# Kernel optimization log

Hardware: AMD Instinct MI355X
Metric: run time of the kernel (lower is better)

## Reference

```python
import jax, jax.numpy as jnp
import numpy as np

D_IN = 1024
D_OUT = 1024
H = 16


def setup_inputs() -> dict:
    key = jax.random.key(0)
    ks = jax.random.split(key, 11)
    B, Tq, Tk = 2, 2048, 2048
    s = 1.0 / np.sqrt(D_IN)
    return {
        "q": jax.random.normal(ks[0], (B, Tq, D_IN), jnp.float32),
        "k": jax.random.normal(ks[1], (B, Tk, D_IN), jnp.float32),
        "v": jax.random.normal(ks[2], (B, Tk, D_IN), jnp.float32),
        "Wq": jax.random.uniform(ks[3], (D_IN, D_OUT), jnp.float32, -s, s),
        "bq": jax.random.uniform(ks[4], (D_OUT,), jnp.float32, -s, s),
        "Wk": jax.random.uniform(ks[5], (D_IN, D_OUT), jnp.float32, -s, s),
        "bk": jax.random.uniform(ks[6], (D_OUT,), jnp.float32, -s, s),
        "Wv": jax.random.uniform(ks[7], (D_IN, D_OUT), jnp.float32, -s, s),
        "bv": jax.random.uniform(ks[8], (D_OUT,), jnp.float32, -s, s),
        "Wo": jax.random.uniform(ks[9], (D_OUT, D_OUT), jnp.float32, -s, s),
        "bo": jax.random.uniform(ks[10], (D_OUT,), jnp.float32, -s, s),
    }


def reference(q, k, v, Wq, bq, Wk, bk, Wv, bv, Wo, bo):
    B, Tq, _ = q.shape
    Tk = k.shape[1]
    hd = D_OUT // H
    # QKV projections, split heads -> [B, H, T, hd]
    qh = (q @ Wq + bq).reshape(B, Tq, H, hd).transpose(0, 2, 1, 3)
    kh = (k @ Wk + bk).reshape(B, Tk, H, hd).transpose(0, 2, 1, 3)
    vh = (v @ Wv + bv).reshape(B, Tk, H, hd).transpose(0, 2, 1, 3)
    # scaled dot-product attention (scale uses key dim = head_dim)
    scores = jnp.einsum("bhqd,bhkd->bhqk", qh, kh) / jnp.sqrt(jnp.float32(hd))
    attn = jax.nn.softmax(scores, axis=-1)
    x = jnp.einsum("bhqk,bhkd->bhqd", attn, vh)
    x = x.transpose(0, 2, 1, 3).reshape(B, Tq, D_OUT)
    return x @ Wo + bo
```

## Files before the change

kernel.cpp:

```cpp
#include <hip/hip_runtime.h>
#include <hip/hip_bf16.h>

typedef __attribute__((ext_vector_type(8))) short short8;
typedef __attribute__((ext_vector_type(4))) short short4v;
typedef __attribute__((ext_vector_type(4))) float f32x4;

__device__ __forceinline__ unsigned short f2bf(float f) {
    __hip_bfloat16 h = __float2bfloat16(f);
    unsigned short u;
    __builtin_memcpy(&u, &h, 2);
    return u;
}
__device__ __forceinline__ short4v pack4bf(float a, float b, float c, float d) {
    union { unsigned u[2]; short4v s; } r;
    r.u[0] = ((unsigned)f2bf(b) << 16) | f2bf(a);
    r.u[1] = ((unsigned)f2bf(d) << 16) | f2bf(c);
    return r.s;
}

#define GLD16(gp, lp) __builtin_amdgcn_global_load_lds( \
    (const __attribute__((address_space(1))) void*)(gp), \
    (__attribute__((address_space(3))) void*)(lp), 16, 0, 0)

__global__ __launch_bounds__(256) void prep(
    const float* __restrict__ q, const float* __restrict__ k, const float* __restrict__ v,
    unsigned short* __restrict__ qb, unsigned short* __restrict__ kb, unsigned short* __restrict__ vb,
    const float* __restrict__ W0, const float* __restrict__ W1,
    const float* __restrict__ W2, const float* __restrict__ W3,
    unsigned short* __restrict__ T0, unsigned short* __restrict__ T1,
    unsigned short* __restrict__ T2, unsigned short* __restrict__ T3)
{
    __shared__ unsigned short Ts[64 * 72];
    int bx = blockIdx.x;
    if (bx < 6144) {
        const float* src; unsigned short* dst;
        switch (bx >> 11) { case 0: src = q; dst = qb; break;
                            case 1: src = k; dst = kb; break;
                            default: src = v; dst = vb; break; }
        size_t i = ((size_t)(bx & 2047) * 256 + threadIdx.x) * 8;
        float4 x0 = *(const float4*)&src[i];
        float4 x1 = *(const float4*)&src[i + 4];
        union { unsigned short s[8]; uint4 u; } p;
        p.s[0] = f2bf(x0.x); p.s[1] = f2bf(x0.y); p.s[2] = f2bf(x0.z); p.s[3] = f2bf(x0.w);
        p.s[4] = f2bf(x1.x); p.s[5] = f2bf(x1.y); p.s[6] = f2bf(x1.z); p.s[7] = f2bf(x1.w);
        *(uint4*)&dst[i] = p.u;
        return;
    }
    int w = bx - 6144;
    int z = w >> 8, rem = w & 255;
    int kx = rem >> 4, ny = rem & 15;
    const float* W;
    unsigned short* T;
    switch (z) {
        case 0: W = W0; T = T0; break;
        case 1: W = W1; T = T1; break;
        case 2: W = W2; T = T2; break;
        default: W = W3; T = T3; break;
    }
    int tid = threadIdx.x;
    int c = tid & 7, r = tid >> 3;
    int k0 = kx * 64, n0 = ny * 64;
    for (int i = 0; i < 64; i += 32) {
        const float* src = &W[(size_t)(k0 + r + i) * 1024 + n0 + c * 8];
        float4 x0 = *(const float4*)src;
        float4 x1 = *(const float4*)(src + 4);
        unsigned short* d = &Ts[(r + i) * 72 + c * 8];
        d[0] = f2bf(x0.x); d[1] = f2bf(x0.y); d[2] = f2bf(x0.z); d[3] = f2bf(x0.w);
        d[4] = f2bf(x1.x); d[5] = f2bf(x1.y); d[6] = f2bf(x1.z); d[7] = f2bf(x1.w);
    }
    __syncthreads();
    for (int i = 0; i < 64; i += 32) {
        union { unsigned short s[8]; uint4 v; } u;
        for (int j = 0; j < 8; j++) u.s[j] = Ts[(c * 8 + j) * 72 + (r + i)];
        *(uint4*)&T[(size_t)(n0 + r + i) * 1024 + k0 + c * 8] = u.v;
    }
}

__device__ __forceinline__ void gemm_core(
    const unsigned short* __restrict__ A, const unsigned short* __restrict__ BT,
    const float* __restrict__ bias, void* __restrict__ outv,
    int mode, float scale)
{
    const int K = 1024;
    __shared__ unsigned short As[128 * 32];
    __shared__ unsigned short Bs[128 * 32];
    int tid = threadIdx.x;
    int m0 = blockIdx.x * 128, n0 = blockIdx.y * 128;
    int lane = tid & 63, wave = tid >> 6;
    int lm = lane & 15, quad = lane >> 4;
    int wm = (wave >> 1) * 64, wn = (wave & 1) * 64;

    int lrow = lane >> 2;
    int scol = ((lane & 3) ^ ((lane >> 3) & 3)) * 8;
    const unsigned short* Ag = A + (size_t)(m0 + wave * 32 + lrow) * K + scol;
    const unsigned short* Bg = BT + (size_t)(n0 + wave * 32 + lrow) * K + scol;
    unsigned short* AsW0 = &As[(wave * 32) * 32];
    unsigned short* AsW1 = &As[(wave * 32 + 16) * 32];
    unsigned short* BsW0 = &Bs[(wave * 32) * 32];
    unsigned short* BsW1 = &Bs[(wave * 32 + 16) * 32];

    int rpos = (quad ^ ((lm >> 1) & 3)) * 8;

    f32x4 acc[4][4];
    for (int i = 0; i < 4; i++)
        for (int j = 0; j < 4; j++)
            for (int r = 0; r < 4; r++) acc[i][j][r] = 0.0f;

    for (int kb = 0; kb < K; kb += 32) {
        GLD16(Ag, AsW0);
        GLD16(Ag + 16 * K, AsW1);
        GLD16(Bg, BsW0);
        GLD16(Bg + 16 * K, BsW1);
        Ag += 32; Bg += 32;
        __syncthreads();
        short8 a[4], b[4];
        for (int i = 0; i < 4; i++)
            a[i] = *(const short8*)&As[(wm + i * 16 + lm) * 32 + rpos];
        for (int j = 0; j < 4; j++)
            b[j] = *(const short8*)&Bs[(wn + j * 16 + lm) * 32 + rpos];
        for (int i = 0; i < 4; i++)
            for (int j = 0; j < 4; j++)
                acc[i][j] = __builtin_amdgcn_mfma_f32_16x16x32_bf16(a[i], b[j], acc[i][j], 0, 0, 0);
        __syncthreads();
    }

    for (int j = 0; j < 4; j++) {
        int col = n0 + wn + j * 16 + lm;
        float bv = bias[col];
        for (int i = 0; i < 4; i++) {
            int rowb = m0 + wm + i * 16 + quad * 4;
            if (mode == 0) {
                float* out32 = (float*)outv;
                for (int r = 0; r < 4; r++)
                    out32[(size_t)(rowb + r) * 1024 + col] = (acc[i][j][r] + bv) * scale;
            } else if (mode == 1) {
                unsigned short* out16 = (unsigned short*)outv;
                int h = col >> 6, d = col & 63;
                int bb = rowb >> 11, t = rowb & 2047;
                size_t base = (((size_t)(bb * 16 + h)) * 2048 + t) * 64 + d;
                for (int r = 0; r < 4; r++)
                    out16[base + (size_t)r * 64] = f2bf((acc[i][j][r] + bv) * scale);
            } else {
                unsigned short* out16 = (unsigned short*)outv;
                int h = col >> 6, d = col & 63;
                int bb = rowb >> 11, t = rowb & 2047;
                ushort4 pk;
                pk.x = f2bf((acc[i][j][0] + bv) * scale);
                pk.y = f2bf((acc[i][j][1] + bv) * scale);
                pk.z = f2bf((acc[i][j][2] + bv) * scale);
                pk.w = f2bf((acc[i][j][3] + bv) * scale);
                *(ushort4*)&out16[(((size_t)(bb * 16 + h)) * 64 + d) * 2048 + t] = pk;
            }
        }
    }
}

__global__ __launch_bounds__(256) void qkv_gemm(
    const unsigned short* __restrict__ qbf, const unsigned short* __restrict__ kbf,
    const unsigned short* __restrict__ vbf,
    const unsigned short* __restrict__ WqT, const unsigned short* __restrict__ WkT,
    const unsigned short* __restrict__ WvT,
    const float* __restrict__ bq, const float* __restrict__ bk, const float* __restrict__ bv,
    unsigned short* __restrict__ Qh, unsigned short* __restrict__ Kh,
    unsigned short* __restrict__ VhT)
{
    switch (blockIdx.z) {
        case 0:  gemm_core(qbf, WqT, bq, Qh,  1, 0.18033688011f); break;
        case 1:  gemm_core(kbf, WkT, bk, Kh,  1, 1.0f);           break;
        default: gemm_core(vbf, WvT, bv, VhT, 2, 1.0f);           break;
    }
}

__global__ __launch_bounds__(256) void out_gemm(
    const unsigned short* __restrict__ X, const unsigned short* __restrict__ WoT,
    const float* __restrict__ bo, float* __restrict__ out)
{
    gemm_core(X, WoT, bo, out, 0, 1.0f);
}

__global__ __launch_bounds__(256) void attn_kernel(
    const unsigned short* __restrict__ Qh, const unsigned short* __restrict__ Kh,
    const unsigned short* __restrict__ VhT, unsigned short* __restrict__ X)
{
    __shared__ unsigned short Ks[2][64 * 64];
    __shared__ unsigned short Vt[2][64 * 64];

    int tid = threadIdx.x;
    int qb = blockIdx.x & 31, bh = blockIdx.x >> 5;
    int b = bh >> 4, h = bh & 15;
    int lane = tid & 63, wave = tid >> 6;
    int lm = lane & 15, quad = lane >> 4;

    const unsigned short* Kbase = Kh + (size_t)bh * 2048 * 64;
    const unsigned short* Vbase = VhT + (size_t)bh * 64 * 2048;

    int srow = wave * 8 + (lane >> 3);
    int schk = ((lane & 7) ^ ((lane >> 3) & 7)) * 8;
    int swz  = lm & 7;
    int c0 = (quad ^ swz) * 8;
    int c1 = ((quad + 4) ^ swz) * 8;

    int qrow = qb * 64 + wave * 16 + lm;
    const unsigned short* qptr = Qh + ((size_t)bh * 2048 + qrow) * 64;
    short8 qf0 = *(const short8*)&qptr[quad * 8];
    short8 qf1 = *(const short8*)&qptr[32 + quad * 8];

    f32x4 o[4];
    for (int n = 0; n < 4; n++)
        for (int r = 0; r < 4; r++) o[n][r] = 0.0f;
    float l = 0.0f;

    GLD16(&Kbase[(size_t)srow * 64 + schk],          &Ks[0][(wave * 8) * 64]);
    GLD16(&Kbase[(size_t)(32 + srow) * 64 + schk],   &Ks[0][(32 + wave * 8) * 64]);
    GLD16(&Vbase[(size_t)srow * 2048 + schk],        &Vt[0][(wave * 8) * 64]);
    GLD16(&Vbase[(size_t)(32 + srow) * 2048 + schk], &Vt[0][(32 + wave * 8) * 64]);
    __syncthreads();

    for (int kt = 0; kt < 32; kt++) {
        int cur = kt & 1;
        if (kt < 31) {
            int k1 = (kt + 1) * 64;
            int nxt = cur ^ 1;
            GLD16(&Kbase[(size_t)(k1 + srow) * 64 + schk],        &Ks[nxt][(wave * 8) * 64]);
            GLD16(&Kbase[(size_t)(k1 + 32 + srow) * 64 + schk],   &Ks[nxt][(32 + wave * 8) * 64]);
            GLD16(&Vbase[(size_t)srow * 2048 + k1 + schk],        &Vt[nxt][(wave * 8) * 64]);
            GLD16(&Vbase[(size_t)(32 + srow) * 2048 + k1 + schk], &Vt[nxt][(32 + wave * 8) * 64]);
        }

        short4v pa[4];
        for (int t = 0; t < 4; t++) {
            short8 ka0 = *(const short8*)&Ks[cur][(t * 16 + lm) * 64 + c0];
            short8 ka1 = *(const short8*)&Ks[cur][(t * 16 + lm) * 64 + c1];
            f32x4 z;
            z[0] = z[1] = z[2] = z[3] = 0.0f;
            z = __builtin_amdgcn_mfma_f32_16x16x32_bf16(ka0, qf0, z, 0, 0, 0);
            z = __builtin_amdgcn_mfma_f32_16x16x32_bf16(ka1, qf1, z, 0, 0, 0);
            float p0 = __builtin_amdgcn_exp2f(z[0]);
            float p1 = __builtin_amdgcn_exp2f(z[1]);
            float p2 = __builtin_amdgcn_exp2f(z[2]);
            float p3 = __builtin_amdgcn_exp2f(z[3]);
            l += (p0 + p1) + (p2 + p3);
            pa[t] = pack4bf(p0, p1, p2, p3);
        }

        int wo = (quad & 1) * 4;
        for (int n = 0; n < 4; n++) {
            int rbase = (n * 16 + lm) * 64;
            for (int t = 0; t < 4; t++) {
                int chunk = t * 2 + (quad >> 1);
                short4v vb = *(const short4v*)&Vt[cur][rbase + ((chunk ^ swz) * 8) + wo];
                o[n] = __builtin_amdgcn_mfma_f32_16x16x16bf16_1k(pa[t], vb, o[n], 0, 0, 0);
            }
        }
        __syncthreads();
    }

    l += __shfl_xor(l, 16);
    l += __shfl_xor(l, 32);
    float inv = 1.0f / l;

    for (int r = 0; r < 4; r++) {
        float invr = __shfl(inv, (lane & 48) | (quad * 4 + r));
        int row = qb * 64 + wave * 16 + quad * 4 + r;
        for (int n = 0; n < 4; n++)
            X[((size_t)b * 2048 + row) * 1024 + h * 64 + n * 16 + lm] = f2bf(o[n][r] * invr);
    }
}

extern "C" void kernel_launch(void* const* d_in, const int* in_sizes, int n_in,
                              void* d_out, int out_size, void* d_ws, size_t ws_size,
                              hipStream_t stream)
{
    const float* q  = (const float*)d_in[0];
    const float* k  = (const float*)d_in[1];
    const float* v  = (const float*)d_in[2];
    const float* Wq = (const float*)d_in[3];
    const float* bq = (const float*)d_in[4];
    const float* Wk = (const float*)d_in[5];
    const float* bk = (const float*)d_in[6];
    const float* Wv = (const float*)d_in[7];
    const float* bv = (const float*)d_in[8];
    const float* Wo = (const float*)d_in[9];
    const float* bo = (const float*)d_in[10];

    unsigned short* ws  = (unsigned short*)d_ws;
    const unsigned int M1 = 1u << 20;
    unsigned short* WqT = ws;
    unsigned short* WkT = ws + M1;
    unsigned short* WvT = ws + 2 * M1;
    unsigned short* WoT = ws + 3 * M1;
    unsigned short* qbf = ws + 4 * M1;
    unsigned short* kbf = ws + 8 * M1;
    unsigned short* vbf = ws + 12 * M1;
    unsigned short* Qh  = ws + 16 * M1;
    unsigned short* Kh  = ws + 4 * M1;
    unsigned short* VhT = ws + 8 * M1;
    unsigned short* X   = ws + 12 * M1;

    prep<<<dim3(7168), 256, 0, stream>>>(q, k, v, qbf, kbf, vbf,
                                         Wq, Wk, Wv, Wo, WqT, WkT, WvT, WoT);
    qkv_gemm<<<dim3(32, 8, 3), 256, 0, stream>>>(qbf, kbf, vbf, WqT, WkT, WvT,
                                                 bq, bk, bv, Qh, Kh, VhT);
    attn_kernel<<<dim3(1024), 256, 0, stream>>>(Qh, Kh, VhT, X);
    out_gemm<<<dim3(32, 8), 256, 0, stream>>>(X, WoT, bo, (float*)d_out);
}
```

Baseline: 235.6 us.

## Double per-wave query rows in attention and vectorize GEMM epilogue stores

The attention kernel now handles 128 query rows per block (32 per wave, as two 16-row sub-tiles), so each K/V tile loaded into shared memory is reused across twice as many queries and the grid is halved. Separately, the GEMM swaps MFMA operand order for modes 0 and 1 so each lane holds four consecutive columns. That lets the epilogue use float4 bias loads and float4/ushort4 vector stores instead of scalar strided stores. The cost is more registers per wave in attention and fewer blocks to fill the GPU.

After: 252.1 us. 7.0% more time.

```diff
diff --git a/kernel.cpp b/kernel.cpp
--- a/kernel.cpp
+++ b/kernel.cpp
@@ -118,30 +118,57 @@
             a[i] = *(const short8*)&As[(wm + i * 16 + lm) * 32 + rpos];
         for (int j = 0; j < 4; j++)
             b[j] = *(const short8*)&Bs[(wn + j * 16 + lm) * 32 + rpos];
-        for (int i = 0; i < 4; i++)
-            for (int j = 0; j < 4; j++)
-                acc[i][j] = __builtin_amdgcn_mfma_f32_16x16x32_bf16(a[i], b[j], acc[i][j], 0, 0, 0);
+        if (mode == 2) {
+            for (int i = 0; i < 4; i++)
+                for (int j = 0; j < 4; j++)
+                    acc[i][j] = __builtin_amdgcn_mfma_f32_16x16x32_bf16(a[i], b[j], acc[i][j], 0, 0, 0);
+        } else {
+            for (int i = 0; i < 4; i++)
+                for (int j = 0; j < 4; j++)
+                    acc[i][j] = __builtin_amdgcn_mfma_f32_16x16x32_bf16(b[j], a[i], acc[i][j], 0, 0, 0);
+        }
         __syncthreads();
     }
 
-    for (int j = 0; j < 4; j++) {
-        int col = n0 + wn + j * 16 + lm;
-        float bv = bias[col];
-        for (int i = 0; i < 4; i++) {
-            int rowb = m0 + wm + i * 16 + quad * 4;
-            if (mode == 0) {
-                float* out32 = (float*)outv;
-                for (int r = 0; r < 4; r++)
-                    out32[(size_t)(rowb + r) * 1024 + col] = (acc[i][j][r] + bv) * scale;
-            } else if (mode == 1) {
-                unsigned short* out16 = (unsigned short*)outv;
-                int h = col >> 6, d = col & 63;
-                int bb = rowb >> 11, t = rowb & 2047;
-                size_t base = (((size_t)(bb * 16 + h)) * 2048 + t) * 64 + d;
-                for (int r = 0; r < 4; r++)
-                    out16[base + (size_t)r * 64] = f2bf((acc[i][j][r] + bv) * scale);
-            } else {
-                unsigned short* out16 = (unsigned short*)outv;
+    if (mode == 0) {
+        float* out32 = (float*)outv;
+        for (int j = 0; j < 4; j++) {
+            int cbase = n0 + wn + j * 16 + quad * 4;
+            float4 b4 = *(const float4*)&bias[cbase];
+            for (int i = 0; i < 4; i++) {
+                int row = m0 + wm + i * 16 + lm;
+                float4 st;
+                st.x = (acc[i][j][0] + b4.x) * scale;
+                st.y = (acc[i][j][1] + b4.y) * scale;
+                st.z = (acc[i][j][2] + b4.z) * scale;
+                st.w = (acc[i][j][3] + b4.w) * scale;
+                *(float4*)&out32[(size_t)row * 1024 + cbase] = st;
+            }
+        }
+    } else if (mode == 1) {
+        unsigned short* out16 = (unsigned short*)outv;
+        for (int j = 0; j < 4; j++) {
+            int cbase = n0 + wn + j * 16 + quad * 4;
+            float4 b4 = *(const float4*)&bias[cbase];
+            int h = cbase >> 6, d0 = cbase & 63;
+            for (int i = 0; i < 4; i++) {
+                int rowm = m0 + wm + i * 16 + lm;
+                int bb = rowm >> 11, t = rowm & 2047;
+                ushort4 pk;
+                pk.x = f2bf((acc[i][j][0] + b4.x) * scale);
+                pk.y = f2bf((acc[i][j][1] + b4.y) * scale);
+                pk.z = f2bf((acc[i][j][2] + b4.z) * scale);
+                pk.w = f2bf((acc[i][j][3] + b4.w) * scale);
+                *(ushort4*)&out16[(((size_t)(bb * 16 + h)) * 2048 + t) * 64 + d0] = pk;
+            }
+        }
+    } else {
+        unsigned short* out16 = (unsigned short*)outv;
+        for (int j = 0; j < 4; j++) {
+            int col = n0 + wn + j * 16 + lm;
+            float bv = bias[col];
+            for (int i = 0; i < 4; i++) {
+                int rowb = m0 + wm + i * 16 + quad * 4;
                 int h = col >> 6, d = col & 63;
                 int bb = rowb >> 11, t = rowb & 2047;
                 ushort4 pk;
@@ -186,7 +213,7 @@
     __shared__ unsigned short Vt[2][64 * 64];
 
     int tid = threadIdx.x;
-    int qb = blockIdx.x & 31, bh = blockIdx.x >> 5;
+    int qb = blockIdx.x & 15, bh = blockIdx.x >> 4;
     int b = bh >> 4, h = bh & 15;
     int lane = tid & 63, wave = tid >> 6;
     int lm = lane & 15, quad = lane >> 4;
@@ -200,15 +227,20 @@
     int c0 = (quad ^ swz) * 8;
     int c1 = ((quad + 4) ^ swz) * 8;
 
-    int qrow = qb * 64 + wave * 16 + lm;
-    const unsigned short* qptr = Qh + ((size_t)bh * 2048 + qrow) * 64;
-    short8 qf0 = *(const short8*)&qptr[quad * 8];
-    short8 qf1 = *(const short8*)&qptr[32 + quad * 8];
-
-    f32x4 o[4];
-    for (int n = 0; n < 4; n++)
-        for (int r = 0; r < 4; r++) o[n][r] = 0.0f;
-    float l = 0.0f;
+    int qrow = qb * 128 + wave * 32 + lm;
+    const unsigned short* qptr0 = Qh + ((size_t)bh * 2048 + qrow) * 64;
+    const unsigned short* qptr1 = qptr0 + 16 * 64;
+    short8 qf[2][2];
+    qf[0][0] = *(const short8*)&qptr0[quad * 8];
+    qf[0][1] = *(const short8*)&qptr0[32 + quad * 8];
+    qf[1][0] = *(const short8*)&qptr1[quad * 8];
+    qf[1][1] = *(const short8*)&qptr1[32 + quad * 8];
+
+    f32x4 o[2][4];
+    for (int qs = 0; qs < 2; qs++)
+        for (int n = 0; n < 4; n++)
+            for (int r = 0; r < 4; r++) o[qs][n][r] = 0.0f;
+    float lsum[2] = {0.0f, 0.0f};
 
     GLD16(&Kbase[(size_t)srow * 64 + schk],          &Ks[0][(wave * 8) * 64]);
     GLD16(&Kbase[(size_t)(32 + srow) * 64 + schk],   &Ks[0][(32 + wave * 8) * 64]);
@@ -227,20 +259,22 @@
             GLD16(&Vbase[(size_t)(32 + srow) * 2048 + k1 + schk], &Vt[nxt][(32 + wave * 8) * 64]);
         }
 
-        short4v pa[4];
+        short4v pa[2][4];
         for (int t = 0; t < 4; t++) {
             short8 ka0 = *(const short8*)&Ks[cur][(t * 16 + lm) * 64 + c0];
             short8 ka1 = *(const short8*)&Ks[cur][(t * 16 + lm) * 64 + c1];
-            f32x4 z;
-            z[0] = z[1] = z[2] = z[3] = 0.0f;
-            z = __builtin_amdgcn_mfma_f32_16x16x32_bf16(ka0, qf0, z, 0, 0, 0);
-            z = __builtin_amdgcn_mfma_f32_16x16x32_bf16(ka1, qf1, z, 0, 0, 0);
-            float p0 = __builtin_amdgcn_exp2f(z[0]);
-            float p1 = __builtin_amdgcn_exp2f(z[1]);
-            float p2 = __builtin_amdgcn_exp2f(z[2]);
-            float p3 = __builtin_amdgcn_exp2f(z[3]);
-            l += (p0 + p1) + (p2 + p3);
-            pa[t] = pack4bf(p0, p1, p2, p3);
+            for (int qs = 0; qs < 2; qs++) {
+                f32x4 z;
+                z[0] = z[1] = z[2] = z[3] = 0.0f;
+                z = __builtin_amdgcn_mfma_f32_16x16x32_bf16(ka0, qf[qs][0], z, 0, 0, 0);
+                z = __builtin_amdgcn_mfma_f32_16x16x32_bf16(ka1, qf[qs][1], z, 0, 0, 0);
+                float p0 = __builtin_amdgcn_exp2f(z[0]);
+                float p1 = __builtin_amdgcn_exp2f(z[1]);
+                float p2 = __builtin_amdgcn_exp2f(z[2]);
+                float p3 = __builtin_amdgcn_exp2f(z[3]);
+                lsum[qs] += (p0 + p1) + (p2 + p3);
+                pa[qs][t] = pack4bf(p0, p1, p2, p3);
+            }
         }
 
         int wo = (quad & 1) * 4;
@@ -249,21 +283,24 @@
             for (int t = 0; t < 4; t++) {
                 int chunk = t * 2 + (quad >> 1);
                 short4v vb = *(const short4v*)&Vt[cur][rbase + ((chunk ^ swz) * 8) + wo];
-                o[n] = __builtin_amdgcn_mfma_f32_16x16x16bf16_1k(pa[t], vb, o[n], 0, 0, 0);
+                o[0][n] = __builtin_amdgcn_mfma_f32_16x16x16bf16_1k(pa[0][t], vb, o[0][n], 0, 0, 0);
+                o[1][n] = __builtin_amdgcn_mfma_f32_16x16x16bf16_1k(pa[1][t], vb, o[1][n], 0, 0, 0);
             }
         }
         __syncthreads();
     }
 
-    l += __shfl_xor(l, 16);
-    l += __shfl_xor(l, 32);
-    float inv = 1.0f / l;
-
-    for (int r = 0; r < 4; r++) {
-        float invr = __shfl(inv, (lane & 48) | (quad * 4 + r));
-        int row = qb * 64 + wave * 16 + quad * 4 + r;
-        for (int n = 0; n < 4; n++)
-            X[((size_t)b * 2048 + row) * 1024 + h * 64 + n * 16 + lm] = f2bf(o[n][r] * invr);
+    for (int qs = 0; qs < 2; qs++) {
+        float l = lsum[qs];
+        l += __shfl_xor(l, 16);
+        l += __shfl_xor(l, 32);
+        float inv = 1.0f / l;
+        for (int r = 0; r < 4; r++) {
+            float invr = __shfl(inv, (lane & 48) | (quad * 4 + r));
+            int row = qb * 128 + wave * 32 + qs * 16 + quad * 4 + r;
+            for (int n = 0; n < 4; n++)
+                X[((size_t)b * 2048 + row) * 1024 + h * 64 + n * 16 + lm] = f2bf(o[qs][n][r] * invr);
+        }
     }
 }
 
@@ -301,6 +338,6 @@
                                          Wq, Wk, Wv, Wo, WqT, WkT, WvT, WoT);
     qkv_gemm<<<dim3(32, 8, 3), 256, 0, stream>>>(qbf, kbf, vbf, WqT, WkT, WvT,
                                                  bq, bk, bv, Qh, Kh, VhT);
-    attn_kernel<<<dim3(1024), 256, 0, stream>>>(Qh, Kh, VhT, X);
+    attn_kernel<<<dim3(512), 256, 0, stream>>>(Qh, Kh, VhT, X);
     out_gemm<<<dim3(32, 8), 256, 0, stream>>>(X, WoT, bo, (float*)d_out);
 }
```
